# Kernel tuning notes

Measured on AMD Instinct MI355X. Metric: run time of the kernel, lower is better.

## Reference

```python
import jax, jax.numpy as jnp
import numpy as np

B, L, D, MAXW = 8, 512, 768, 12
H = D // 2  # forward/backward half of the bidirectional encoder output


def setup_inputs() -> dict:
    key = jax.random.key(0)
    k1, k2, k3, k4 = jax.random.split(key, 4)
    h = jax.random.normal(k1, (B, L, D), jnp.float32)
    # ATG-style span enumeration: start=i, end=min(i+w, L-1) for w in [0, MAXW)
    starts = jnp.broadcast_to(jnp.arange(L)[:, None], (L, MAXW))
    ends = jnp.minimum(starts + jnp.arange(MAXW)[None, :], L - 1)
    span_idx = jnp.stack([starts, ends], axis=-1).reshape(1, L * MAXW, 2)
    span_idx = jnp.broadcast_to(span_idx, (B, L * MAXW, 2)).astype(jnp.int64)
    # downproject: Linear(D -> D) since BidirectionalEndpointSpanExtractor output dim == D
    W = jax.random.normal(k2, (D, D), jnp.float32) / np.sqrt(D)
    b = jnp.zeros((D,), jnp.float32)
    # learned sentinels (use_sentinels=True default), one per half
    start_sentinel = jax.random.normal(k3, (H,), jnp.float32) * 0.02
    end_sentinel = jax.random.normal(k4, (H,), jnp.float32) * 0.02
    return {"h": h, "span_idx": span_idx, "W": W, "b": b,
            "start_sentinel": start_sentinel, "end_sentinel": end_sentinel}


def _gather(seq, idx):
    # seq: (B, L, H), idx: (B, S) -> (B, S, H)
    return jnp.take_along_axis(seq, idx[..., None], axis=1)


def reference(h, span_idx, W, b, start_sentinel, end_sentinel):
    Bv, Lv, Dv = h.shape
    Hv = Dv // 2
    fwd, bwd = h[..., :Hv], h[..., Hv:]
    starts = span_idx[..., 0]
    ends = span_idx[..., 1]
    # exclusive endpoints
    excl_starts = starts - 1
    start_mask = excl_starts == -1                 # before sequence start -> start sentinel
    excl_ends = ends + 1
    end_mask = excl_ends >= Lv                     # past sequence end -> end sentinel
    excl_starts = jnp.where(start_mask, 0, excl_starts)
    excl_ends = jnp.where(end_mask, 0, excl_ends)
    f_start = _gather(fwd, excl_starts)            # (B, S, H)
    f_end = _gather(fwd, ends)
    b_start = _gather(bwd, excl_ends)
    b_end = _gather(bwd, starts)
    f_start = jnp.where(start_mask[..., None], start_sentinel, f_start)
    b_start = jnp.where(end_mask[..., None], end_sentinel, b_start)
    # forward_combination='y-x', backward_combination='x-y'
    span_rep = jnp.concatenate([f_end - f_start, b_start - b_end], axis=-1)  # (B, S, D)
    out = jax.nn.relu(jnp.einsum('bsd,ed->bse', span_rep, W) + b)
    return out.reshape(Bv, Lv, -1, Dv)            # (B, L, MAXW, D)
```

## Files before the change

### kernel.cpp

```cpp
#include <hip/hip_runtime.h>

typedef __attribute__((ext_vector_type(4))) float f32x4;
typedef __attribute__((ext_vector_type(8))) _Float16 f16x8;
typedef __attribute__((ext_vector_type(4))) unsigned short u16x4;

#define NB 8
#define LLEN 512
#define DD 768
#define MW 12
#define HH 384
#define TT (NB * LLEN)
#define SS (LLEN * MW)
#define RB 528
#define MX (NB * RB)

#define BT 32
#define BE 128
#define WR 48
#define PR 136

#define PREPX_BLOCKS ((MX * 192) / 256)
#define PREPW_BLOCKS ((DD * 192) / 256)
#define PREP_BLOCKS (PREPX_BLOCKS + PREPW_BLOCKS)

__device__ __forceinline__ unsigned short f2h(float x) {
  _Float16 h = (_Float16)x;
  return __builtin_bit_cast(unsigned short, h);
}
__device__ __forceinline__ float h2f(unsigned short u) {
  return (float)__builtin_bit_cast(_Float16, u);
}
__device__ __forceinline__ void gload_lds16(const void* g, void* l) {
  __builtin_amdgcn_global_load_lds(
      (const __attribute__((address_space(1))) unsigned int*)g,
      (__attribute__((address_space(3))) unsigned int*)l, 16, 0, 0);
}

__global__ __launch_bounds__(256) void prep_k(const float* __restrict__ h,
                                              const float* __restrict__ W,
                                              const float* __restrict__ ss,
                                              const float* __restrict__ es,
                                              unsigned short* __restrict__ X,
                                              unsigned short* __restrict__ Wp) {
  int bid = blockIdx.x;
  if (bid < PREPX_BLOCKS) {
    int idx = bid * 256 + threadIdx.x;
    int r = idx / 192;
    int c = (idx - r * 192) * 4;
    int b = r / RB;
    int t = r - b * RB - 1;
    const float* src;
    if (c < HH) {
      src = (t == -1) ? (ss + c) : (h + ((size_t)b * LLEN + min(t, LLEN - 1)) * DD + c);
    } else {
      src = (t >= LLEN - 1) ? (es + (c - HH))
                            : (h + ((size_t)b * LLEN + (t + 1)) * DD + c);
    }
    f32x4 f = *(const f32x4*)src;
    u16x4 v;
#pragma unroll
    for (int j = 0; j < 4; ++j) v[j] = f2h(f[j]);
    *(u16x4*)(X + (size_t)r * DD + c) = v;
  } else {
    int idx = (bid - PREPX_BLOCKS) * 256 + threadIdx.x;
    int e = idx / 192;
    int c = (idx - e * 192) * 4;
    f32x4 f = *(const f32x4*)(W + (size_t)e * DD + c);
    u16x4 v;
#pragma unroll
    for (int j = 0; j < 4; ++j) v[j] = f2h(f[j]);
    *(u16x4*)(Wp + (size_t)e * DD + c) = v;
  }
}

__global__ __launch_bounds__(256) void fused_k(const unsigned short* __restrict__ X,
                                               const unsigned short* __restrict__ Wp,
                                               const int* __restrict__ span,
                                               const float* __restrict__ bias,
                                               float* __restrict__ out) {
  __shared__ char lds[WR * 128 + BE * 128];
  __shared__ int2 spans[BT * MW];

  const int bid = blockIdx.x;
  const int g = ((bid >> 3) / 6) * 8 + (bid & 7);
  const int ec = (bid >> 3) % 6;
  const int b = g >> 4;
  const int T0 = (g & 15) * BT;
  const int E0 = ec * BE;

  const int tid = threadIdx.x;
  const int lane = tid & 63;
  const int wc = tid >> 6;
  const int l16 = lane & 15, l4 = lane >> 4;

  {
    const int2* sp = (const int2*)span + (size_t)b * SS + (size_t)T0 * MW;
    for (int s = tid; s < BT * MW; s += 256) spans[s] = sp[s];
  }

  char* As = lds;
  char* Bs = lds + WR * 128;

  const size_t xbase = (size_t)b * RB + T0;
  const char* Xb = (const char*)X;
  const char* Wb = (const char*)Wp;

  f32x4 acc[3][2] = {};

  for (int kc = 0; kc < DD; kc += 64) {
    {
      int o = tid * 16;
      int rr = o >> 7, cb = o & 127;
      gload_lds16(Xb + ((xbase + rr) * DD + kc) * 2 + cb, As + o);
    }
    if (tid < 128) {
      int o = 4096 + tid * 16;
      int rr = o >> 7, cb = o & 127;
      gload_lds16(Xb + ((xbase + rr) * DD + kc) * 2 + cb, As + o);
    }
#pragma unroll
    for (int r = 0; r < 4; ++r) {
      int o = (r * 256 + tid) * 16;
      int rr = o >> 7, cb = o & 127;
      gload_lds16(Wb + ((size_t)(E0 + rr) * DD + kc) * 2 + cb, Bs + o);
    }
    __syncthreads();

    f16x8 af[2][3], bf[2][2];
#pragma unroll
    for (int ks = 0; ks < 2; ++ks)
#pragma unroll
      for (int m = 0; m < 3; ++m)
        af[ks][m] = *(const f16x8*)(As + (m * 16 + l16) * 128 + ks * 64 + l4 * 16);
#pragma unroll
    for (int ks = 0; ks < 2; ++ks)
#pragma unroll
      for (int n = 0; n < 2; ++n)
        bf[ks][n] = *(const f16x8*)(Bs + (wc * 32 + n * 16 + l16) * 128 + ks * 64 + l4 * 16);

#pragma unroll
    for (int m = 0; m < 3; ++m)
#pragma unroll
      for (int n = 0; n < 2; ++n) {
        acc[m][n] = __builtin_amdgcn_mfma_f32_16x16x32_f16(af[0][m], bf[0][n], acc[m][n], 0, 0, 0);
        acc[m][n] = __builtin_amdgcn_mfma_f32_16x16x32_f16(af[1][m], bf[1][n], acc[m][n], 0, 0, 0);
      }
    __syncthreads();
  }

  unsigned short* Rt = (unsigned short*)lds;
#pragma unroll
  for (int m = 0; m < 3; ++m) {
    int row = m * 16 + l4 * 4;
#pragma unroll
    for (int n = 0; n < 2; ++n) {
      int col = wc * 32 + n * 16 + l16;
#pragma unroll
      for (int r = 0; r < 4; ++r)
        Rt[(row + r) * PR + col] = f2h(acc[m][n][r]);
    }
  }
  __syncthreads();

  const u16x4* R4 = (const u16x4*)Rt;
  const f32x4* bias4 = (const f32x4*)bias + (E0 >> 2);
  f32x4* out4 = (f32x4*)out + ((size_t)b * SS + (size_t)T0 * MW) * (DD / 4) + (E0 >> 2);

  const int e4 = tid & 31;
  int lw = tid >> 5;
  const f32x4 bb = bias4[e4];
#pragma unroll 4
  for (int it = 0; it < (BT * MW) / 8; ++it) {
    const int2 se = spans[lw];
    u16x4 pe = R4[(se.y - T0 + 1) * 34 + e4];
    u16x4 mq = R4[(se.x - T0) * 34 + e4];
    f32x4 r;
#pragma unroll
    for (int j = 0; j < 4; ++j) {
      float x = h2f(pe[j]) - h2f(mq[j]) + bb[j];
      r[j] = fmaxf(x, 0.f);
    }
    out4[(size_t)lw * (DD / 4) + e4] = r;
    lw += 8;
  }
}

__global__ __launch_bounds__(256) void naive_k(const float* __restrict__ h,
                                               const int* __restrict__ span,
                                               const float* __restrict__ W,
                                               const float* __restrict__ bias,
                                               const float* __restrict__ ss,
                                               const float* __restrict__ es,
                                               float* __restrict__ out) {
  int bs = blockIdx.x;
  int b = bs / SS;
  int start = span[(size_t)bs * 2 + 0];
  int end   = span[(size_t)bs * 2 + 1];
  __shared__ float rep[DD];
  const float* hb = h + (size_t)b * LLEN * DD;
  for (int k = threadIdx.x; k < HH; k += blockDim.x) {
    float fs = (start == 0) ? ss[k] : hb[(size_t)(start - 1) * DD + k];
    rep[k] = hb[(size_t)end * DD + k] - fs;
    float bstart = (end + 1 >= LLEN) ? es[k] : hb[(size_t)(end + 1) * DD + HH + k];
    rep[HH + k] = bstart - hb[(size_t)start * DD + HH + k];
  }
  __syncthreads();
  for (int e = threadIdx.x; e < DD; e += blockDim.x) {
    const float* w = W + (size_t)e * DD;
    float acc = bias[e];
    for (int k = 0; k < DD; k += 4) {
      acc += rep[k] * w[k] + rep[k + 1] * w[k + 1] + rep[k + 2] * w[k + 2] + rep[k + 3] * w[k + 3];
    }
    out[(size_t)bs * DD + e] = fmaxf(acc, 0.f);
  }
}

extern "C" void kernel_launch(void* const* d_in, const int* in_sizes, int n_in,
                              void* d_out, int out_size, void* d_ws, size_t ws_size,
                              hipStream_t stream) {
  const float* h  = (const float*)d_in[0];
  const int* span = (const int*)d_in[1];
  const float* W  = (const float*)d_in[2];
  const float* bias = (const float*)d_in[3];
  const float* ss = (const float*)d_in[4];
  const float* es = (const float*)d_in[5];
  float* out = (float*)d_out;

  const size_t szX = (size_t)MX * DD * sizeof(unsigned short);
  const size_t szW = (size_t)DD * DD * sizeof(unsigned short);
  const size_t need = szX + szW;

  if (ws_size < need) {
    naive_k<<<NB * SS, 256, 0, stream>>>(h, span, W, bias, ss, es, out);
    return;
  }

  char* ws = (char*)d_ws;
  unsigned short* X  = (unsigned short*)ws;
  unsigned short* Wp = X + (size_t)MX * DD;

  prep_k<<<PREP_BLOCKS, 256, 0, stream>>>(h, W, ss, es, X, Wp);
  fused_k<<<768, 256, 0, stream>>>(X, Wp, span, bias, out);
}
```

Baseline: 48.88 us.

## Process two row tiles per block, overlapping first tile's output writes with second GEMM

```diff
diff --git a/kernel.cpp b/kernel.cpp
--- a/kernel.cpp
+++ b/kernel.cpp
@@ -15,9 +15,9 @@
 #define MX (NB * RB)
 
 #define BT 32
-#define BE 128
+#define BE 64
 #define WR 48
-#define PR 136
+#define PRF 68
 
 #define PREPX_BLOCKS ((MX * 192) / 256)
 #define PREPW_BLOCKS ((DD * 192) / 256)
@@ -26,9 +26,6 @@
 __device__ __forceinline__ unsigned short f2h(float x) {
   _Float16 h = (_Float16)x;
   return __builtin_bit_cast(unsigned short, h);
-}
-__device__ __forceinline__ float h2f(unsigned short u) {
-  return (float)__builtin_bit_cast(_Float16, u);
 }
 __device__ __forceinline__ void gload_lds16(const void* g, void* l) {
   __builtin_amdgcn_global_load_lds(
@@ -73,116 +70,127 @@
   }
 }
 
-__global__ __launch_bounds__(256) void fused_k(const unsigned short* __restrict__ X,
-                                               const unsigned short* __restrict__ Wp,
-                                               const int* __restrict__ span,
-                                               const float* __restrict__ bias,
-                                               float* __restrict__ out) {
-  __shared__ char lds[WR * 128 + BE * 128];
-  __shared__ int2 spans[BT * MW];
+__global__ __launch_bounds__(256, 3) void fused_k(const unsigned short* __restrict__ X,
+                                                  const unsigned short* __restrict__ Wp,
+                                                  const int* __restrict__ span,
+                                                  const float* __restrict__ bias,
+                                                  float* __restrict__ out) {
+  __shared__ char stg[6144 + 8192];
+  __shared__ float Rt0[WR * PRF];
+  __shared__ float Rt1[WR * PRF];
+  __shared__ int2 spans[2 * BT * MW];
 
   const int bid = blockIdx.x;
-  const int g = ((bid >> 3) / 6) * 8 + (bid & 7);
-  const int ec = (bid >> 3) % 6;
-  const int b = g >> 4;
-  const int T0 = (g & 15) * BT;
+  const int ec = bid >> 6;
+  const int p  = bid & 63;
+  const int b  = p >> 3;
+  const int T0 = (p & 7) * (2 * BT);
   const int E0 = ec * BE;
 
   const int tid = threadIdx.x;
   const int lane = tid & 63;
-  const int wc = tid >> 6;
+  const int wv = tid >> 6;
   const int l16 = lane & 15, l4 = lane >> 4;
 
   {
     const int2* sp = (const int2*)span + (size_t)b * SS + (size_t)T0 * MW;
-    for (int s = tid; s < BT * MW; s += 256) spans[s] = sp[s];
-  }
-
-  char* As = lds;
-  char* Bs = lds + WR * 128;
-
-  const size_t xbase = (size_t)b * RB + T0;
+    for (int s = tid; s < 2 * BT * MW; s += 256) spans[s] = sp[s];
+  }
+
+  char* As = stg;
+  char* Bs = stg + 6144;
   const char* Xb = (const char*)X;
   const char* Wb = (const char*)Wp;
-
-  f32x4 acc[3][2] = {};
-
-  for (int kc = 0; kc < DD; kc += 64) {
-    {
-      int o = tid * 16;
-      int rr = o >> 7, cb = o & 127;
-      gload_lds16(Xb + ((xbase + rr) * DD + kc) * 2 + cb, As + o);
-    }
-    if (tid < 128) {
-      int o = 4096 + tid * 16;
-      int rr = o >> 7, cb = o & 127;
-      gload_lds16(Xb + ((xbase + rr) * DD + kc) * 2 + cb, As + o);
-    }
-#pragma unroll
-    for (int r = 0; r < 4; ++r) {
-      int o = (r * 256 + tid) * 16;
-      int rr = o >> 7, cb = o & 127;
-      gload_lds16(Wb + ((size_t)(E0 + rr) * DD + kc) * 2 + cb, Bs + o);
-    }
-    __syncthreads();
-
-    f16x8 af[2][3], bf[2][2];
-#pragma unroll
-    for (int ks = 0; ks < 2; ++ks)
-#pragma unroll
-      for (int m = 0; m < 3; ++m)
-        af[ks][m] = *(const f16x8*)(As + (m * 16 + l16) * 128 + ks * 64 + l4 * 16);
-#pragma unroll
-    for (int ks = 0; ks < 2; ++ks)
-#pragma unroll
-      for (int n = 0; n < 2; ++n)
-        bf[ks][n] = *(const f16x8*)(Bs + (wc * 32 + n * 16 + l16) * 128 + ks * 64 + l4 * 16);
-
-#pragma unroll
-    for (int m = 0; m < 3; ++m)
-#pragma unroll
-      for (int n = 0; n < 2; ++n) {
-        acc[m][n] = __builtin_amdgcn_mfma_f32_16x16x32_f16(af[0][m], bf[0][n], acc[m][n], 0, 0, 0);
-        acc[m][n] = __builtin_amdgcn_mfma_f32_16x16x32_f16(af[1][m], bf[1][n], acc[m][n], 0, 0, 0);
-      }
-    __syncthreads();
-  }
-
-  unsigned short* Rt = (unsigned short*)lds;
-#pragma unroll
-  for (int m = 0; m < 3; ++m) {
-    int row = m * 16 + l4 * 4;
-#pragma unroll
-    for (int n = 0; n < 2; ++n) {
-      int col = wc * 32 + n * 16 + l16;
-#pragma unroll
-      for (int r = 0; r < 4; ++r)
-        Rt[(row + r) * PR + col] = f2h(acc[m][n][r]);
-    }
-  }
+  const size_t xb0 = (size_t)b * RB + T0;
+  const size_t xb1 = xb0 + BT;
+
+  const int e4 = tid & 15;
+  const int lw0 = tid >> 4;
+  const f32x4 bb = ((const f32x4*)bias)[(E0 >> 2) + e4];
+  f32x4* outB = (f32x4*)out + ((size_t)b * SS + (size_t)T0 * MW) * (DD / 4) + (E0 >> 2);
+
+#define STAGE(xbase, kc)                                                      \
+  {                                                                           \
+    { int o = tid * 16; int rr = o >> 7, cb = o & 127;                        \
+      gload_lds16(Xb + (((xbase) + rr) * DD + (kc)) * 2 + cb, As + o); }      \
+    if (tid < 128) { int o = 4096 + tid * 16; int rr = o >> 7, cb = o & 127;  \
+      gload_lds16(Xb + (((xbase) + rr) * DD + (kc)) * 2 + cb, As + o); }      \
+    _Pragma("unroll")                                                         \
+    for (int r2 = 0; r2 < 2; ++r2) {                                          \
+      int o = (r2 * 256 + tid) * 16; int rr = o >> 7, cb = o & 127;           \
+      gload_lds16(Wb + ((size_t)(E0 + rr) * DD + (kc)) * 2 + cb, Bs + o);     \
+    }                                                                         \
+  }
+
+#define COMPUTE(acc)                                                          \
+  {                                                                           \
+    f16x8 af[2][3], bf[2];                                                    \
+    _Pragma("unroll")                                                         \
+    for (int ks = 0; ks < 2; ++ks) {                                          \
+      _Pragma("unroll")                                                       \
+      for (int m = 0; m < 3; ++m)                                             \
+        af[ks][m] = *(const f16x8*)(As + (m * 16 + l16) * 128 + ks * 64 + l4 * 16); \
+      bf[ks] = *(const f16x8*)(Bs + (wv * 16 + l16) * 128 + ks * 64 + l4 * 16);     \
+    }                                                                         \
+    _Pragma("unroll")                                                         \
+    for (int m = 0; m < 3; ++m) {                                             \
+      acc[m] = __builtin_amdgcn_mfma_f32_16x16x32_f16(af[0][m], bf[0], acc[m], 0, 0, 0); \
+      acc[m] = __builtin_amdgcn_mfma_f32_16x16x32_f16(af[1][m], bf[1], acc[m], 0, 0, 0); \
+    }                                                                         \
+  }
+
+#define ACC2LDS(acc, Rt)                                                      \
+  _Pragma("unroll")                                                           \
+  for (int m = 0; m < 3; ++m) {                                               \
+    int row = m * 16 + l4 * 4;                                                \
+    _Pragma("unroll")                                                         \
+    for (int r = 0; r < 4; ++r)                                               \
+      (Rt)[(row + r) * PRF + wv * 16 + l16] = acc[m][r];                      \
+  }
+
+#define WITER(Rt, w, it)                                                      \
+  {                                                                           \
+    int lw = lw0 + (it) * 16;                                                 \
+    int2 se = spans[(w) * BT * MW + lw];                                      \
+    int tb = T0 + (w) * BT;                                                   \
+    const f32x4* R4 = (const f32x4*)(Rt);                                     \
+    f32x4 pe = R4[(se.y - tb + 1) * (PRF / 4) + e4];                          \
+    f32x4 mq = R4[(se.x - tb) * (PRF / 4) + e4];                              \
+    f32x4 rr;                                                                 \
+    _Pragma("unroll")                                                         \
+    for (int j = 0; j < 4; ++j) rr[j] = fmaxf(pe[j] - mq[j] + bb[j], 0.f);    \
+    outB[((size_t)(w) * BT * MW + lw) * (DD / 4) + e4] = rr;                  \
+  }
+
+  f32x4 acc0[3] = {};
+  for (int ki = 0; ki < 12; ++ki) {
+    STAGE(xb0, ki * 64);
+    __syncthreads();
+    COMPUTE(acc0);
+    __syncthreads();
+  }
+  ACC2LDS(acc0, Rt0);
   __syncthreads();
 
-  const u16x4* R4 = (const u16x4*)Rt;
-  const f32x4* bias4 = (const f32x4*)bias + (E0 >> 2);
-  f32x4* out4 = (f32x4*)out + ((size_t)b * SS + (size_t)T0 * MW) * (DD / 4) + (E0 >> 2);
-
-  const int e4 = tid & 31;
-  int lw = tid >> 5;
-  const f32x4 bb = bias4[e4];
+  f32x4 acc1[3] = {};
+  for (int ki = 0; ki < 12; ++ki) {
+    STAGE(xb1, ki * 64);
+    WITER(Rt0, 0, 2 * ki);
+    WITER(Rt0, 0, 2 * ki + 1);
+    __syncthreads();
+    COMPUTE(acc1);
+    __syncthreads();
+  }
+  ACC2LDS(acc1, Rt1);
+  __syncthreads();
+
 #pragma unroll 4
-  for (int it = 0; it < (BT * MW) / 8; ++it) {
-    const int2 se = spans[lw];
-    u16x4 pe = R4[(se.y - T0 + 1) * 34 + e4];
-    u16x4 mq = R4[(se.x - T0) * 34 + e4];
-    f32x4 r;
-#pragma unroll
-    for (int j = 0; j < 4; ++j) {
-      float x = h2f(pe[j]) - h2f(mq[j]) + bb[j];
-      r[j] = fmaxf(x, 0.f);
-    }
-    out4[(size_t)lw * (DD / 4) + e4] = r;
-    lw += 8;
-  }
+  for (int it = 0; it < 24; ++it) WITER(Rt1, 1, it);
+
+#undef STAGE
+#undef COMPUTE
+#undef ACC2LDS
+#undef WITER
 }
 
 __global__ __launch_bounds__(256) void naive_k(const float* __restrict__ h,
```

Result: no change. 48.92 us (+0.1%).

## Load GEMM fragments directly from global and keep per-wave fp32 epilogue tiles

Applied to the files above, without the earlier changes.

```diff
diff --git a/kernel.cpp b/kernel.cpp
--- a/kernel.cpp
+++ b/kernel.cpp
@@ -16,8 +16,7 @@
 
 #define BT 32
 #define BE 128
-#define WR 48
-#define PR 136
+#define PRT 36
 
 #define PREPX_BLOCKS ((MX * 192) / 256)
 #define PREPW_BLOCKS ((DD * 192) / 256)
@@ -26,14 +25,6 @@
 __device__ __forceinline__ unsigned short f2h(float x) {
   _Float16 h = (_Float16)x;
   return __builtin_bit_cast(unsigned short, h);
-}
-__device__ __forceinline__ float h2f(unsigned short u) {
-  return (float)__builtin_bit_cast(_Float16, u);
-}
-__device__ __forceinline__ void gload_lds16(const void* g, void* l) {
-  __builtin_amdgcn_global_load_lds(
-      (const __attribute__((address_space(1))) unsigned int*)g,
-      (__attribute__((address_space(3))) unsigned int*)l, 16, 0, 0);
 }
 
 __global__ __launch_bounds__(256) void prep_k(const float* __restrict__ h,
@@ -73,12 +64,12 @@
   }
 }
 
-__global__ __launch_bounds__(256) void fused_k(const unsigned short* __restrict__ X,
-                                               const unsigned short* __restrict__ Wp,
-                                               const int* __restrict__ span,
-                                               const float* __restrict__ bias,
-                                               float* __restrict__ out) {
-  __shared__ char lds[WR * 128 + BE * 128];
+__global__ __launch_bounds__(256, 3) void fused_k(const unsigned short* __restrict__ X,
+                                                  const unsigned short* __restrict__ Wp,
+                                                  const int* __restrict__ span,
+                                                  const float* __restrict__ bias,
+                                                  float* __restrict__ out) {
+  __shared__ float Rt[4][48 * PRT];
   __shared__ int2 spans[BT * MW];
 
   const int bid = blockIdx.x;
@@ -90,54 +81,32 @@
 
   const int tid = threadIdx.x;
   const int lane = tid & 63;
-  const int wc = tid >> 6;
+  const int wv = tid >> 6;
   const int l16 = lane & 15, l4 = lane >> 4;
 
   {
     const int2* sp = (const int2*)span + (size_t)b * SS + (size_t)T0 * MW;
     for (int s = tid; s < BT * MW; s += 256) spans[s] = sp[s];
   }
-
-  char* As = lds;
-  char* Bs = lds + WR * 128;
-
-  const size_t xbase = (size_t)b * RB + T0;
-  const char* Xb = (const char*)X;
-  const char* Wb = (const char*)Wp;
+  __syncthreads();
+
+  const unsigned short* Xw = X + ((size_t)b * RB + T0) * DD;
+  const unsigned short* Wn = Wp + (size_t)(E0 + wv * 32) * DD;
 
   f32x4 acc[3][2] = {};
-
-  for (int kc = 0; kc < DD; kc += 64) {
-    {
-      int o = tid * 16;
-      int rr = o >> 7, cb = o & 127;
-      gload_lds16(Xb + ((xbase + rr) * DD + kc) * 2 + cb, As + o);
+#pragma unroll 4
+  for (int ki = 0; ki < 12; ++ki) {
+    const int kc = ki * 64;
+    f16x8 af[2][3], bf[2][2];
+#pragma unroll
+    for (int ks = 0; ks < 2; ++ks) {
+#pragma unroll
+      for (int m = 0; m < 3; ++m)
+        af[ks][m] = *(const f16x8*)&Xw[(size_t)(m * 16 + l16) * DD + kc + ks * 32 + l4 * 8];
+#pragma unroll
+      for (int n = 0; n < 2; ++n)
+        bf[ks][n] = *(const f16x8*)&Wn[(size_t)(n * 16 + l16) * DD + kc + ks * 32 + l4 * 8];
     }
-    if (tid < 128) {
-      int o = 4096 + tid * 16;
-      int rr = o >> 7, cb = o & 127;
-      gload_lds16(Xb + ((xbase + rr) * DD + kc) * 2 + cb, As + o);
-    }
-#pragma unroll
-    for (int r = 0; r < 4; ++r) {
-      int o = (r * 256 + tid) * 16;
-      int rr = o >> 7, cb = o & 127;
-      gload_lds16(Wb + ((size_t)(E0 + rr) * DD + kc) * 2 + cb, Bs + o);
-    }
-    __syncthreads();
-
-    f16x8 af[2][3], bf[2][2];
-#pragma unroll
-    for (int ks = 0; ks < 2; ++ks)
-#pragma unroll
-      for (int m = 0; m < 3; ++m)
-        af[ks][m] = *(const f16x8*)(As + (m * 16 + l16) * 128 + ks * 64 + l4 * 16);
-#pragma unroll
-    for (int ks = 0; ks < 2; ++ks)
-#pragma unroll
-      for (int n = 0; n < 2; ++n)
-        bf[ks][n] = *(const f16x8*)(Bs + (wc * 32 + n * 16 + l16) * 128 + ks * 64 + l4 * 16);
-
 #pragma unroll
     for (int m = 0; m < 3; ++m)
 #pragma unroll
@@ -145,43 +114,33 @@
         acc[m][n] = __builtin_amdgcn_mfma_f32_16x16x32_f16(af[0][m], bf[0][n], acc[m][n], 0, 0, 0);
         acc[m][n] = __builtin_amdgcn_mfma_f32_16x16x32_f16(af[1][m], bf[1][n], acc[m][n], 0, 0, 0);
       }
-    __syncthreads();
-  }
-
-  unsigned short* Rt = (unsigned short*)lds;
-#pragma unroll
-  for (int m = 0; m < 3; ++m) {
-    int row = m * 16 + l4 * 4;
-#pragma unroll
-    for (int n = 0; n < 2; ++n) {
-      int col = wc * 32 + n * 16 + l16;
+  }
+
+  float* Rw = Rt[wv];
+#pragma unroll
+  for (int m = 0; m < 3; ++m)
+#pragma unroll
+    for (int n = 0; n < 2; ++n)
 #pragma unroll
       for (int r = 0; r < 4; ++r)
-        Rt[(row + r) * PR + col] = f2h(acc[m][n][r]);
-    }
-  }
-  __syncthreads();
-
-  const u16x4* R4 = (const u16x4*)Rt;
-  const f32x4* bias4 = (const f32x4*)bias + (E0 >> 2);
-  f32x4* out4 = (f32x4*)out + ((size_t)b * SS + (size_t)T0 * MW) * (DD / 4) + (E0 >> 2);
-
-  const int e4 = tid & 31;
-  int lw = tid >> 5;
-  const f32x4 bb = bias4[e4];
+        Rw[(m * 16 + l4 * 4 + r) * PRT + n * 16 + l16] = acc[m][n][r];
+
+  const int e4 = lane & 7;
+  const int lr = lane >> 3;
+  const f32x4 bb = ((const f32x4*)bias)[(E0 + wv * 32) / 4 + e4];
+  f32x4* outB = (f32x4*)out + ((size_t)b * SS + (size_t)T0 * MW) * (DD / 4)
+              + (E0 + wv * 32) / 4 + e4;
+
 #pragma unroll 4
-  for (int it = 0; it < (BT * MW) / 8; ++it) {
+  for (int it = 0; it < 48; ++it) {
+    const int lw = it * 8 + lr;
     const int2 se = spans[lw];
-    u16x4 pe = R4[(se.y - T0 + 1) * 34 + e4];
-    u16x4 mq = R4[(se.x - T0) * 34 + e4];
-    f32x4 r;
-#pragma unroll
-    for (int j = 0; j < 4; ++j) {
-      float x = h2f(pe[j]) - h2f(mq[j]) + bb[j];
-      r[j] = fmaxf(x, 0.f);
-    }
-    out4[(size_t)lw * (DD / 4) + e4] = r;
-    lw += 8;
+    f32x4 pe = *(const f32x4*)&Rw[(se.y - T0 + 1) * PRT + e4 * 4];
+    f32x4 mq = *(const f32x4*)&Rw[(se.x - T0) * PRT + e4 * 4];
+    f32x4 rr;
+#pragma unroll
+    for (int j = 0; j < 4; ++j) rr[j] = fmaxf(pe[j] - mq[j] + bb[j], 0.f);
+    outB[(size_t)lw * (DD / 4)] = rr;
   }
 }
 
```

Result: slower. 75.09 us (+53.6%).
